# Performance work log

Hardware: AMD Instinct MI355X
Metric: run time of the kernel (lower is better)

The kernel has to match this reference:

```python
import jax, jax.numpy as jnp
import numpy as np

B, C, T = 4, 768, 512
H, KS, NL, W = 12, 3, 6, 4
D = C // H  # 64


def setup_inputs() -> dict:
    key = jax.random.key(0)
    ks = jax.random.split(key, 24)
    def n(k, shape, scale):
        return jax.random.normal(k, shape, dtype=jnp.float32) * scale
    cscale = C ** -0.5
    return {
        "x": jax.random.normal(ks[0], (B, C, T), dtype=jnp.float32),
        "x_mask": jnp.ones((B, 1, T), dtype=jnp.float32),
        "Wq": n(ks[1], (NL, C, C), cscale), "bq": jnp.zeros((NL, C), jnp.float32),
        "Wk": n(ks[2], (NL, C, C), cscale), "bk": jnp.zeros((NL, C), jnp.float32),
        "Wv": n(ks[3], (NL, C, C), cscale), "bv": jnp.zeros((NL, C), jnp.float32),
        "Wo": n(ks[4], (NL, C, C), cscale), "bo": jnp.zeros((NL, C), jnp.float32),
        "emb_rel_k": n(ks[5], (NL, D, 2 * W + 1), D ** -0.5),
        "emb_rel_v": n(ks[6], (NL, D, 2 * W + 1), D ** -0.5),
        "ffn_w1": n(ks[7], (NL, 4 * C, C, KS), (C * KS) ** -0.5),
        "ffn_b1": jnp.zeros((NL, 4 * C), jnp.float32),
        "ffn_w2": n(ks[8], (NL, C, 4 * C, KS), (4 * C * KS) ** -0.5),
        "ffn_b2": jnp.zeros((NL, C), jnp.float32),
        "norm1_g": jnp.ones((NL, C), jnp.float32), "norm1_b": jnp.zeros((NL, C), jnp.float32),
        "norm2_g": jnp.ones((NL, C), jnp.float32), "norm2_b": jnp.zeros((NL, C), jnp.float32),
    }


def _conv1x1(x, w, b):  # x:[B,C,T] w:[O,C] -> [B,O,T]
    return jnp.einsum('oc,bct->bot', w, x) + b[None, :, None]


def _conv1d(x, w, b, pad):  # x:[B,Ci,T] w:[O,Ci,K]
    y = jax.lax.conv_general_dilated(x, w, (1,), [(pad, pad)],
                                     dimension_numbers=('NCH', 'OIH', 'NCH'))
    return y + b[None, :, None]


def _layer_norm_c(x, g, b):  # normalize over channel dim of [B,C,T]
    m = jnp.mean(x, axis=1, keepdims=True)
    v = jnp.var(x, axis=1, keepdims=True)
    return (x - m) * jax.lax.rsqrt(v + 1e-5) * g[None, :, None] + b[None, :, None]


def _rel_to_abs(x):  # [b,h,l,2l-1] -> [b,h,l,l]
    b, h, l, _ = x.shape
    x = jnp.pad(x, ((0, 0), (0, 0), (0, 0), (0, 1)))
    x = x.reshape(b, h, l * 2 * l)
    x = jnp.pad(x, ((0, 0), (0, 0), (0, l - 1)))
    return x.reshape(b, h, l + 1, 2 * l - 1)[:, :, :l, l - 1:]


def _abs_to_rel(x):  # [b,h,l,l] -> [b,h,l,2l-1]
    b, h, l, _ = x.shape
    x = jnp.pad(x, ((0, 0), (0, 0), (0, 0), (0, l - 1)))
    x = x.reshape(b, h, l * l + l * (l - 1))
    x = jnp.pad(x, ((0, 0), (0, 0), (l, 0)))
    return x.reshape(b, h, l, 2 * l)[:, :, :, 1:]


def _get_rel_emb(emb, t, w):  # emb:[D,2w+1] -> [D,2t-1]
    pad = max(t - (w + 1), 0)
    start = max(w + 1 - t, 0)
    e = jnp.pad(emb, ((0, 0), (pad, pad)))
    return e[:, start:start + 2 * t - 1]


def _attention(x, attn_mask, wq, bq, wk, bk, wv, bv, wo, bo, ek, ev):
    b, c, t = x.shape
    scale = D ** 0.5
    q = _conv1x1(x, wq, bq).reshape(b, H, D, t)
    k = _conv1x1(x, wk, bk).reshape(b, H, D, t)
    v = _conv1x1(x, wv, bv).reshape(b, H, D, t)
    scores = jnp.einsum('bhdt,bhds->bhts', q, k) / scale  # [b,H,t,t]
    k_emb = _get_rel_emb(ek, t, W)  # [D,2t-1]
    rel_logits = jnp.einsum('bhdt,dr->bhtr', q / scale, k_emb)
    scores = scores + _rel_to_abs(rel_logits)
    scores = jnp.where(attn_mask == 0, -10000.0, scores)
    p = jax.nn.softmax(scores, axis=-1)
    out = jnp.einsum('bhts,bhds->bhdt', p, v)
    v_emb = _get_rel_emb(ev, t, W)  # [D,2t-1]
    out = out + jnp.einsum('bhtr,dr->bhdt', _abs_to_rel(p), v_emb)
    return _conv1x1(out.reshape(b, c, t), wo, bo)


def _ffn(x, x_mask, w1, b1, w2, b2):
    y = _conv1d(x * x_mask, w1, b1, KS // 2)
    y = jax.nn.gelu(y, approximate=False)
    y = _conv1d(y * x_mask, w2, b2, KS // 2)
    return y * x_mask


def reference(x, x_mask, Wq, bq, Wk, bk, Wv, bv, Wo, bo, emb_rel_k, emb_rel_v,
              ffn_w1, ffn_b1, ffn_w2, ffn_b2, norm1_g, norm1_b, norm2_g, norm2_b):
    attn_mask = x_mask[:, :, None, :] * x_mask[:, :, :, None]  # [B,1,T,T]
    for i in range(NL):
        y = _attention(x, attn_mask, Wq[i], bq[i], Wk[i], bk[i], Wv[i], bv[i],
                       Wo[i], bo[i], emb_rel_k[i], emb_rel_v[i])
        x = _layer_norm_c(x + y, norm1_g[i], norm1_b[i])
        y = _ffn(x, x_mask, ffn_w1[i], ffn_b1[i], ffn_w2[i], ffn_b2[i])
        x = _layer_norm_c(x + y, norm2_g[i], norm2_b[i])
        x = x * x_mask
    return x
```

## Files before the change

kernel.cpp:

```cpp
#include <hip/hip_runtime.h>
#include <cstddef>

namespace {

constexpr int B  = 4;
constexpr int C  = 768;
constexpr int T  = 512;
constexpr int H  = 12;
constexpr int D  = 64;
constexpr int NL = 6;
constexpr int W  = 4;
constexpr int FF = 3072;

typedef __attribute__((ext_vector_type(8))) short sh8;
typedef __attribute__((ext_vector_type(4))) float f32x4;

__device__ inline float gelu_exact(float x) {
  return 0.5f * x * (1.0f + erff(x * 0.70710678118654752440f));
}
__device__ inline unsigned short f2b(float f) {
  unsigned u = __float_as_uint(f);
  unsigned r = (u + 0x7fffu + ((u >> 16) & 1u)) >> 16;
  return (unsigned short)r;
}
__device__ inline float b2f(unsigned short u) {
  return __uint_as_float((unsigned)u << 16);
}
__device__ inline void gload_lds16(const void* g, void* l) {
  __builtin_amdgcn_global_load_lds(
      (const __attribute__((address_space(1))) unsigned int*)g,
      (__attribute__((address_space(3))) unsigned int*)l, 16, 0, 0);
}

__global__ __launch_bounds__(256) void transpose_cvt_in(
    const float* __restrict__ s, unsigned short* __restrict__ dh,
    float* __restrict__ df)
{
  __shared__ float tile[32][33];
  const int b = blockIdx.z;
  const int c0 = blockIdx.y * 32, t0 = blockIdx.x * 32;
  const int tx = threadIdx.x & 31, ty = threadIdx.x >> 5;
  const float* sp = s + ((size_t)b * C + c0) * T + t0;
#pragma unroll
  for (int i = 0; i < 4; ++i)
    tile[ty + i * 8][tx] = sp[(size_t)(ty + i * 8) * T + tx];
  __syncthreads();
  unsigned short* dph = dh + ((size_t)b * T + t0) * C + c0;
  float* dpf = df + ((size_t)b * T + t0) * C + c0;
#pragma unroll
  for (int i = 0; i < 4; ++i) {
    const float v = tile[tx][ty + i * 8];
    dph[(size_t)(ty + i * 8) * C + tx] = f2b(v);
    dpf[(size_t)(ty + i * 8) * C + tx] = v;
  }
}

__global__ __launch_bounds__(256) void transpose_out(
    const float* __restrict__ s, float* __restrict__ d)
{
  __shared__ float tile[32][33];
  const int b = blockIdx.z;
  const int c0 = blockIdx.y * 32, t0 = blockIdx.x * 32;
  const int tx = threadIdx.x & 31, ty = threadIdx.x >> 5;
  const float* sp = s + ((size_t)b * T + t0) * C + c0;
#pragma unroll
  for (int i = 0; i < 4; ++i)
    tile[ty + i * 8][tx] = sp[(size_t)(ty + i * 8) * C + tx];
  __syncthreads();
  float* dp = d + ((size_t)b * C + c0) * T + t0;
#pragma unroll
  for (int i = 0; i < 4; ++i)
    dp[(size_t)(ty + i * 8) * T + tx] = tile[tx][ty + i * 8];
}

__global__ __launch_bounds__(256) void cvt_qkvo_tiled(
    const float* __restrict__ q, const float* __restrict__ k,
    const float* __restrict__ v, const float* __restrict__ o,
    unsigned short* __restrict__ dq, unsigned short* __restrict__ dk,
    unsigned short* __restrict__ dv, unsigned short* __restrict__ dov)
{
  __shared__ float lds[16][132];
  const int z = blockIdx.y;
  const size_t loff = (size_t)blockIdx.z * C * C;
  const float* s = (z == 0 ? q : z == 1 ? k : z == 2 ? v : o) + loff;
  unsigned short* d = (z == 0 ? dq : z == 1 ? dk : z == 2 ? dv : dov) + loff;
  constexpr int KST = C / 32;
  constexpr int KSG = KST / 4;
  const int mt = blockIdx.x / KSG;
  const int ksg = blockIdx.x % KSG;
  const int tid = threadIdx.x;
#pragma unroll
  for (int p = 0; p < 2; ++p) {
    const int f = tid + p * 256;
    const int row = f >> 5, c4 = f & 31;
    f32x4 vv = __builtin_nontemporal_load(
        (const f32x4*)(s + (size_t)(mt * 16 + row) * C + ksg * 128 + c4 * 4));
    *(f32x4*)&lds[row][c4 * 4] = vv;
  }
  __syncthreads();
  const int ksl = tid >> 6, lane = tid & 63;
  const int l15 = lane & 15, lhi = lane >> 4;
  float4 a = *(const float4*)&lds[l15][ksl * 32 + lhi * 8];
  float4 b = *(const float4*)&lds[l15][ksl * 32 + lhi * 8 + 4];
  sh8 u;
  u[0] = (short)f2b(a.x); u[1] = (short)f2b(a.y);
  u[2] = (short)f2b(a.z); u[3] = (short)f2b(a.w);
  u[4] = (short)f2b(b.x); u[5] = (short)f2b(b.y);
  u[6] = (short)f2b(b.z); u[7] = (short)f2b(b.w);
  *(sh8*)(d + ((size_t)(mt * KST + ksg * 4 + ksl) * 64 + lane) * 8) = u;
}

__global__ __launch_bounds__(256) void cvt_ffn_tiled(
    const float* __restrict__ s1, const float* __restrict__ s2,
    unsigned short* __restrict__ d1, unsigned short* __restrict__ d2)
{
  __shared__ float lds[16][388];
  const int z = blockIdx.y;
  const int layer = blockIdx.z;
  const float* src = (z ? s2 : s1) + (size_t)layer * FF * C * 3;
  unsigned short* dst = (z ? d2 : d1) + (size_t)layer * 3 * FF * C;
  const int O  = z ? C : FF;
  const int Ci = z ? FF : C;
  const int KST = Ci >> 5;
  const int KSG = KST >> 2;
  const int mt = blockIdx.x / KSG;
  const int ksg = blockIdx.x % KSG;
  const int tid = threadIdx.x;
  const size_t rowlen = (size_t)Ci * 3;
#pragma unroll
  for (int p = 0; p < 6; ++p) {
    const int f = tid + p * 256;
    const int row = f / 96, c4 = f % 96;
    f32x4 vv = __builtin_nontemporal_load(
        (const f32x4*)(src + (size_t)(mt * 16 + row) * rowlen + ksg * 384 + c4 * 4));
    *(f32x4*)&lds[row][c4 * 4] = vv;
  }
  __syncthreads();
  const int ksl = tid >> 6, lane = tid & 63;
  const int l15 = lane & 15, lhi = lane >> 4;
  const int q0 = ksl * 96 + lhi * 24;
  float f[24];
#pragma unroll
  for (int kq = 0; kq < 6; ++kq) {
    float4 t4 = *(const float4*)&lds[l15][q0 + kq * 4];
    f[kq * 4 + 0] = t4.x; f[kq * 4 + 1] = t4.y;
    f[kq * 4 + 2] = t4.z; f[kq * 4 + 3] = t4.w;
  }
  const size_t fragoff = ((size_t)(mt * KST + ksg * 4 + ksl) * 64 + lane) * 8;
#pragma unroll
  for (int tap = 0; tap < 3; ++tap) {
    sh8 u;
#pragma unroll
    for (int j = 0; j < 8; ++j) u[j] = (short)f2b(f[j * 3 + tap]);
    *(sh8*)(dst + (size_t)tap * O * Ci + fragoff) = u;
  }
}

template <int TAPS, int BN, int KSPLIT, bool GELU, bool MASK_OUT, bool OBF16,
          bool KBIN, bool KBOUT>
__global__ __launch_bounds__(256) void mfma_conv(
    const unsigned short* __restrict__ xin,
    const unsigned short* __restrict__ w0p, const unsigned short* __restrict__ w1p,
    const unsigned short* __restrict__ w2p,
    const float* __restrict__ b0, const float* __restrict__ b1,
    const float* __restrict__ b2,
    const float* __restrict__ mask,
    void* __restrict__ o0p, void* __restrict__ o1p, void* __restrict__ o2p,
    int Cin, int O, int tilesPerPlane, int nz)
{
  constexpr int ROWS_B = BN + TAPS - 1;
  constexpr int PB = 40;
  constexpr int NPASS = BN / 64;
  constexpr int NF = BN / 32;
  constexpr int NT = T / BN;
  __shared__ unsigned short Aw[2][TAPS * 8 * 512];
  __shared__ unsigned short Bx[2][ROWS_B * PB];

  const int nwg = gridDim.x;
  const int orig = blockIdx.x;
  const int wg = (orig & 7) * (nwg >> 3) + (orig >> 3);
  const int txt = wg % NT;
  const int rest = wg / NT;
  const int zz = rest % nz;
  const int ty = rest / nz;

  const int b  = zz / KSPLIT;
  const int kk = zz % KSPLIT;
  const int TOFF = (TAPS == 3) ? -1 : 0;
  const int t0 = txt * BN;
  const int plane = ty / tilesPerPlane;
  const int mt0 = (ty % tilesPerPlane) * 8;
  const int o0 = mt0 * 16;

  const int tid = threadIdx.x;
  const int lane = tid & 63, wid = tid >> 6;
  const int wm = wid >> 1, wn = wid & 1;
  const int l15 = lane & 15, lhi = lane >> 4;
  const int bmask = b * T;

  const unsigned short* wsel = plane == 0 ? w0p : (plane == 1 ? w1p : w2p);
  const float* bp = plane == 0 ? b0 : (plane == 1 ? b1 : b2);

  const int KST = Cin >> 5;
  const int kchunk = KST / KSPLIT;
  const int ks0 = kk * kchunk, ks1 = ks0 + kchunk;
  const int OT = O >> 4;

  const unsigned short* xb_ = xin + (size_t)b * T * Cin;
  const unsigned short* xkb = xin + (size_t)b * KST * T * 32;

  sh8 breg[NPASS], breg2;
  auto stageA = [&](int ks, int buf) {
#pragma unroll
    for (int tap = 0; tap < TAPS; ++tap) {
#pragma unroll
      for (int j = 0; j < 2; ++j) {
        const int rt = wid * 2 + j;
        const unsigned short* src =
            wsel + (((size_t)tap * OT + mt0 + rt) * KST + ks) * 512 + lane * 8;
        gload_lds16(src, &Aw[buf][(tap * 8 + rt) * 512]);
      }
    }
  };
  auto loadB = [&](int ks) {
    const int c0 = ks << 5;
    const unsigned short* kbase = xkb + (size_t)ks * T * 32;
#pragma unroll
    for (int p = 0; p < NPASS; ++p) {
      const int idx = tid + p * 256;
      const int row = idx >> 2, c8 = (idx & 3) << 3;
      const int tsrc = t0 + row + TOFF;
      breg[p] = (sh8)0;
      if ((unsigned)tsrc < (unsigned)T) {
        if constexpr (KBIN)
          breg[p] = *(const sh8*)(kbase + (size_t)tsrc * 32 + c8);
        else
          breg[p] = *(const sh8*)(xb_ + (size_t)tsrc * Cin + c0 + c8);
      }
    }
    if constexpr (TAPS == 3) {
      breg2 = (sh8)0;
      if (tid < 8) {
        const int row = BN + (tid >> 2), c8 = (tid & 3) << 3;
        const int ts2 = t0 + row + TOFF;
        if ((unsigned)ts2 < (unsigned)T) {
          if constexpr (KBIN)
            breg2 = *(const sh8*)(kbase + (size_t)ts2 * 32 + c8);
          else
            breg2 = *(const sh8*)(xb_ + (size_t)ts2 * Cin + c0 + c8);
        }
      }
    }
  };
  auto writeB = [&](int buf) {
#pragma unroll
    for (int p = 0; p < NPASS; ++p) {
      const int idx = tid + p * 256;
      *(sh8*)&Bx[buf][(idx >> 2) * PB + ((idx & 3) << 3)] = breg[p];
    }
    if constexpr (TAPS == 3) {
      if (tid < 8)
        *(sh8*)&Bx[buf][(BN + (tid >> 2)) * PB + ((tid & 3) << 3)] = breg2;
    }
  };

  f32x4 acc[4][NF] = {};

  int cur = 0;
  stageA(ks0, 0);
  loadB(ks0);
  writeB(0);
  __syncthreads();

  for (int ks = ks0; ks < ks1; ++ks) {
    const int nxt = cur ^ 1;
    const bool more = (ks + 1 < ks1);
    if (more) { stageA(ks + 1, nxt); loadB(ks + 1); }
    __builtin_amdgcn_s_setprio(1);
#pragma unroll
    for (int tap = 0; tap < TAPS; ++tap) {
      sh8 af[4], bfr[NF];
#pragma unroll
      for (int m = 0; m < 4; ++m)
        af[m] = *(const sh8*)&Aw[cur][(tap * 8 + wm * 4 + m) * 512 + lane * 8];
#pragma unroll
      for (int n = 0; n < NF; ++n)
        bfr[n] = *(const sh8*)&Bx[cur][(wn * (NF * 16) + n * 16 + l15 + tap) * PB + lhi * 8];
#pragma unroll
      for (int m = 0; m < 4; ++m)
#pragma unroll
        for (int n = 0; n < NF; ++n)
          acc[m][n] = __builtin_amdgcn_mfma_f32_16x16x32_bf16(
              af[m], bfr[n], acc[m][n], 0, 0, 0);
    }
    __builtin_amdgcn_s_setprio(0);
    if (more) writeB(nxt);
    __syncthreads();
    cur = nxt;
  }

  void* obase = plane == 0 ? o0p : (plane == 1 ? o1p : o2p);
  unsigned short* oph = (unsigned short*)obase + (size_t)b * T * O;
  unsigned short* opk = (unsigned short*)obase + (size_t)b * (O >> 5) * T * 32;
  float* opf = (float*)obase + ((size_t)kk * B + b) * (size_t)T * O;
#pragma unroll
  for (int m = 0; m < 4; ++m) {
    const int o = o0 + (wm * 4 + m) * 16 + (lhi << 2);
#pragma unroll
    for (int n = 0; n < NF; ++n) {
      const int t = t0 + wn * (NF * 16) + n * 16 + l15;
      const float mk = MASK_OUT ? mask[bmask + t] : 1.f;
      float v[4];
#pragma unroll
      for (int r4 = 0; r4 < 4; ++r4) {
        float x = acc[m][n][r4];
        if (KSPLIT > 1) {
          if (kk == 0) x += bp[o + r4];
        } else {
          x += bp[o + r4];
        }
        if (GELU) x = gelu_exact(x);
        if (MASK_OUT) x *= mk;
        v[r4] = x;
      }
      if constexpr (OBF16) {
        ushort4 hz;
        hz.x = f2b(v[0]); hz.y = f2b(v[1]); hz.z = f2b(v[2]); hz.w = f2b(v[3]);
        if constexpr (KBOUT)
          *(ushort4*)(opk + ((size_t)(o >> 5) * T + t) * 32 + (o & 31)) = hz;
        else
          *(ushort4*)(oph + (size_t)t * O + o) = hz;
      } else {
        *(float4*)(opf + (size_t)t * O + o) = make_float4(v[0], v[1], v[2], v[3]);
      }
    }
  }
}

__global__ __launch_bounds__(256) void fused_attn(
    const unsigned short* __restrict__ qg,
    const unsigned short* __restrict__ kg,
    const unsigned short* __restrict__ vg,
    const float* __restrict__ mask,
    const float* __restrict__ ek,
    const float* __restrict__ ev,
    unsigned short* __restrict__ outp)
{
  constexpr int PITCH = 72;
  __shared__ unsigned short Qs[64 * PITCH];
  __shared__ unsigned short Ks[2][64 * PITCH];
  __shared__ unsigned short Vs[2][64 * PITCH];
  __shared__ float eks[D * 9], evs[D * 9];
  __shared__ float qekl[64 * 12];
  __shared__ float mks[2][64];
  unsigned short* Ps = Qs;

  const int t0 = blockIdx.x * 64;
  const int bh = blockIdx.y;
  const int b = bh / H, h = bh % H;
  const int tid = threadIdx.x;
  const int lane = tid & 63, w = tid >> 6;
  const int l15 = lane & 15, lhi = lane >> 4;

  const size_t base = (size_t)b * T * C + h * D;
  const unsigned short* qh = qg + base;
  const unsigned short* kh = kg + base;
  const unsigned short* vh = vg + base;

  for (int e = tid; e < D * 9; e += 256) { eks[e] = ek[e]; evs[e] = ev[e]; }
  {
    const int tl = tid & 63, d0 = (tid >> 6) << 4;
    const unsigned short* src = qh + (size_t)(t0 + tl) * C + d0;
    *(sh8*)&Qs[tl * PITCH + d0]     = *(const sh8*)(src);
    *(sh8*)&Qs[tl * PITCH + d0 + 8] = *(const sh8*)(src + 8);
  }
  __syncthreads();
  {
    const int tl = tid & 63, g = tid >> 6;
    for (int j = g; j < 9; j += 4) {
      float a = 0.f;
      for (int d = 0; d < D; ++d)
        a = fmaf(b2f(Qs[tl * PITCH + d]), eks[d * 9 + j], a);
      qekl[tl * 12 + j] = a * 0.125f;
    }
  }
  const int t_loc = w * 16 + l15;
  const int t = t0 + t_loc;
  const float mask_t = mask[b * T + t];
  const sh8 bq0 = *(const sh8*)&Qs[t_loc * PITCH + lhi * 8];
  const sh8 bq1 = *(const sh8*)&Qs[t_loc * PITCH + 32 + lhi * 8];

  const int sl = tid & 63, d0s = (tid >> 6) << 4;
  {
    const unsigned short* srck = kh + (size_t)sl * C + d0s;
    *(sh8*)&Ks[0][sl * PITCH + d0s]     = *(const sh8*)(srck);
    *(sh8*)&Ks[0][sl * PITCH + d0s + 8] = *(const sh8*)(srck + 8);
    const unsigned short* srcv = vh + (size_t)sl * C + d0s;
    sh8 u0 = *(const sh8*)(srcv);
    sh8 u1 = *(const sh8*)(srcv + 8);
#pragma unroll
    for (int j = 0; j < 8; ++j) Vs[0][(d0s + j) * PITCH + sl] = (unsigned short)u0[j];
#pragma unroll
    for (int j = 0; j < 8; ++j) Vs[0][(d0s + 8 + j) * PITCH + sl] = (unsigned short)u1[j];
    if (tid < 64) mks[0][tid] = mask[b * T + tid];
  }
  __syncthreads();

  float m_run = -1e30f, l_run = 0.f;
  f32x4 oacc[4] = {};
  int cur = 0;
  sh8 kr0, kr1, vr0, vr1;
  float mkr = 0.f;

  for (int s0 = 0; s0 < T; s0 += 64) {
    const int nxt = cur ^ 1;
    const bool more = (s0 + 64 < T);
    if (more) {
      const unsigned short* srck = kh + (size_t)(s0 + 64 + sl) * C + d0s;
      kr0 = *(const sh8*)(srck);
      kr1 = *(const sh8*)(srck + 8);
      const unsigned short* srcv = vh + (size_t)(s0 + 64 + sl) * C + d0s;
      vr0 = *(const sh8*)(srcv);
      vr1 = *(const sh8*)(srcv + 8);
      if (tid < 64) mkr = mask[b * T + s0 + 64 + tid];
    }

    float p[16];
#pragma unroll
    for (int n = 0; n < 4; ++n) {
      const sh8 a0 = *(const sh8*)&Ks[cur][(n * 16 + l15) * PITCH + lhi * 8];
      const sh8 a1 = *(const sh8*)&Ks[cur][(n * 16 + l15) * PITCH + 32 + lhi * 8];
      f32x4 acc = {};
      __builtin_amdgcn_s_setprio(1);
      acc = __builtin_amdgcn_mfma_f32_16x16x32_bf16(a0, bq0, acc, 0, 0, 0);
      acc = __builtin_amdgcn_mfma_f32_16x16x32_bf16(a1, bq1, acc, 0, 0, 0);
      __builtin_amdgcn_s_setprio(0);
#pragma unroll
      for (int r = 0; r < 4; ++r) {
        const int s = s0 + n * 16 + lhi * 4 + r;
        float v = acc[r] * 0.125f;
        const int j = s - t + 4;
        if ((unsigned)j < 9u) v += qekl[t_loc * 12 + j];
        if (mask_t * mks[cur][s - s0] == 0.f) v = -10000.0f;
        p[n * 4 + r] = v;
      }
    }
    float mloc = p[0];
#pragma unroll
    for (int i = 1; i < 16; ++i) mloc = fmaxf(mloc, p[i]);
    mloc = fmaxf(mloc, __shfl_xor(mloc, 16));
    mloc = fmaxf(mloc, __shfl_xor(mloc, 32));
    const float m_new = fmaxf(m_run, mloc);
    const float f = __expf(m_run - m_new);
    float sloc = 0.f;
#pragma unroll
    for (int i = 0; i < 16; ++i) { p[i] = __expf(p[i] - m_new); sloc += p[i]; }
    sloc += __shfl_xor(sloc, 16);
    sloc += __shfl_xor(sloc, 32);
    l_run = l_run * f + sloc;
    m_run = m_new;
#pragma unroll
    for (int m = 0; m < 4; ++m)
#pragma unroll
      for (int r = 0; r < 4; ++r) oacc[m][r] *= f;
#pragma unroll
    for (int n = 0; n < 4; ++n) {
      uint2 pk;
      pk.x = (unsigned)f2b(p[n * 4 + 0]) | ((unsigned)f2b(p[n * 4 + 1]) << 16);
      pk.y = (unsigned)f2b(p[n * 4 + 2]) | ((unsigned)f2b(p[n * 4 + 3]) << 16);
      *(uint2*)&Ps[t_loc * PITCH + n * 16 + lhi * 4] = pk;
    }
    asm volatile("s_waitcnt lgkmcnt(0)" ::: "memory");
    const sh8 bp0 = *(const sh8*)&Ps[t_loc * PITCH + lhi * 8];
    const sh8 bp1 = *(const sh8*)&Ps[t_loc * PITCH + 32 + lhi * 8];
    __builtin_amdgcn_s_setprio(1);
#pragma unroll
    for (int m = 0; m < 4; ++m) {
      const sh8 a0 = *(const sh8*)&Vs[cur][(m * 16 + l15) * PITCH + lhi * 8];
      const sh8 a1 = *(const sh8*)&Vs[cur][(m * 16 + l15) * PITCH + 32 + lhi * 8];
      oacc[m] = __builtin_amdgcn_mfma_f32_16x16x32_bf16(a0, bp0, oacc[m], 0, 0, 0);
      oacc[m] = __builtin_amdgcn_mfma_f32_16x16x32_bf16(a1, bp1, oacc[m], 0, 0, 0);
    }
    __builtin_amdgcn_s_setprio(0);
    if (t + 4 >= s0 && t < s0 + 68) {
#pragma unroll
      for (int j = 0; j < 9; ++j) {
        const int s = t + j - 4;
        if (s >= s0 && s < s0 + 64) {
          const float pv = b2f(Ps[t_loc * PITCH + (s - s0)]);
#pragma unroll
          for (int m = 0; m < 4; ++m)
#pragma unroll
            for (int r = 0; r < 4; ++r)
              oacc[m][r] = fmaf(pv, evs[(m * 16 + lhi * 4 + r) * 9 + j], oacc[m][r]);
        }
      }
    }
    if (more) {
      *(sh8*)&Ks[nxt][sl * PITCH + d0s]     = kr0;
      *(sh8*)&Ks[nxt][sl * PITCH + d0s + 8] = kr1;
#pragma unroll
      for (int j = 0; j < 8; ++j) Vs[nxt][(d0s + j) * PITCH + sl] = (unsigned short)vr0[j];
#pragma unroll
      for (int j = 0; j < 8; ++j) Vs[nxt][(d0s + 8 + j) * PITCH + sl] = (unsigned short)vr1[j];
      if (tid < 64) mks[nxt][tid] = mkr;
    }
    __syncthreads();
    cur = nxt;
  }
  const float invl = 1.f / l_run;
  unsigned short* okb = outp + (size_t)b * (C >> 5) * T * 32;
#pragma unroll
  for (int m = 0; m < 4; ++m) {
    ushort4 hz;
    hz.x = f2b(oacc[m][0] * invl);
    hz.y = f2b(oacc[m][1] * invl);
    hz.z = f2b(oacc[m][2] * invl);
    hz.w = f2b(oacc[m][3] * invl);
    const int c = h * D + m * 16 + lhi * 4;
    *(ushort4*)(okb + ((size_t)(c >> 5) * T + t) * 32 + (c & 31)) = hz;
  }
}

template <int NP, bool MASKY, bool MASKF>
__global__ __launch_bounds__(256) void add_norm_wave(
    const float* __restrict__ xr, const float* __restrict__ ypart,
    const float* __restrict__ g, const float* __restrict__ bta,
    const float* __restrict__ mask, float* __restrict__ dst,
    unsigned short* __restrict__ dsth)
{
  const int b = blockIdx.y;
  const int t = blockIdx.x * 4 + (threadIdx.x >> 6);
  const int lane = threadIdx.x & 63;
  const float mkt = mask[b * T + t];
  const size_t rowoff = ((size_t)b * T + t) * C;
  const int ci0 = lane * 12;

  float vv[12];
  float sum = 0.f, sq = 0.f;
#pragma unroll
  for (int q = 0; q < 3; ++q) {
    const int ci = ci0 + q * 4;
    float4 xv = *(const float4*)(xr + rowoff + ci);
    float4 yv = make_float4(0.f, 0.f, 0.f, 0.f);
#pragma unroll
    for (int p = 0; p < NP; ++p) {
      float4 t4 = *(const float4*)(ypart + (size_t)p * B * T * C + rowoff + ci);
      yv.x += t4.x; yv.y += t4.y; yv.z += t4.z; yv.w += t4.w;
    }
    if (MASKY) { yv.x *= mkt; yv.y *= mkt; yv.z *= mkt; yv.w *= mkt; }
    const float v0 = xv.x + yv.x, v1 = xv.y + yv.y;
    const float v2 = xv.z + yv.z, v3 = xv.w + yv.w;
    vv[q * 4 + 0] = v0; vv[q * 4 + 1] = v1; vv[q * 4 + 2] = v2; vv[q * 4 + 3] = v3;
    sum += v0 + v1 + v2 + v3;
    sq = fmaf(v0, v0, fmaf(v1, v1, fmaf(v2, v2, fmaf(v3, v3, sq))));
  }
#pragma unroll
  for (int o = 32; o > 0; o >>= 1) {
    sum += __shfl_xor(sum, o);
    sq += __shfl_xor(sq, o);
  }
  const float m = sum * (1.f / C);
  const float rs = rsqrtf(sq * (1.f / C) - m * m + 1e-5f);
#pragma unroll
  for (int q = 0; q < 3; ++q) {
    const int ci = ci0 + q * 4;
    float4 gv = *(const float4*)(g + ci);
    float4 bv = *(const float4*)(bta + ci);
    float o0 = (vv[q * 4 + 0] - m) * rs * gv.x + bv.x;
    float o1 = (vv[q * 4 + 1] - m) * rs * gv.y + bv.y;
    float o2 = (vv[q * 4 + 2] - m) * rs * gv.z + bv.z;
    float o3 = (vv[q * 4 + 3] - m) * rs * gv.w + bv.w;
    if (MASKF) { o0 *= mkt; o1 *= mkt; o2 *= mkt; o3 *= mkt; }
    *(float4*)(dst + rowoff + ci) = make_float4(o0, o1, o2, o3);
    const float hm = MASKF ? 1.f : mkt;
    ushort4 hz;
    hz.x = f2b(o0 * hm); hz.y = f2b(o1 * hm); hz.z = f2b(o2 * hm); hz.w = f2b(o3 * hm);
    *(ushort4*)(dsth + rowoff + ci) = hz;
  }
}

}

extern "C" void kernel_launch(void* const* d_in, const int* in_sizes, int n_in,
                              void* d_out, int out_size, void* d_ws, size_t ws_size,
                              hipStream_t stream) {
  const float* x_in = (const float*)d_in[0];
  const float* mask = (const float*)d_in[1];
  const float* Wq = (const float*)d_in[2];
  const float* bq = (const float*)d_in[3];
  const float* Wk = (const float*)d_in[4];
  const float* bk = (const float*)d_in[5];
  const float* Wv = (const float*)d_in[6];
  const float* bv = (const float*)d_in[7];
  const float* Wo = (const float*)d_in[8];
  const float* bo = (const float*)d_in[9];
  const float* ek = (const float*)d_in[10];
  const float* ev = (const float*)d_in[11];
  const float* w1 = (const float*)d_in[12];
  const float* b1 = (const float*)d_in[13];
  const float* w2 = (const float*)d_in[14];
  const float* b2 = (const float*)d_in[15];
  const float* n1g = (const float*)d_in[16];
  const float* n1b = (const float*)d_in[17];
  const float* n2g = (const float*)d_in[18];
  const float* n2b = (const float*)d_in[19];

  float* ws = (float*)d_ws;
  const size_t SZ_X = (size_t)B * C * T;
  const size_t SZ_W1 = (size_t)3 * FF * C;
  float* xr    = ws;
  float* xr1   = xr + SZ_X;
  float* ypart = xr1 + SZ_X;
  unsigned short* xbh = (unsigned short*)(ypart + 4 * SZ_X);
  unsigned short* xfh = xbh + SZ_X;
  unsigned short* qbh = xfh + SZ_X;
  unsigned short* kbh = qbh + SZ_X;
  unsigned short* vbh = kbh + SZ_X;
  unsigned short* hidh = vbh + SZ_X;
  unsigned short* w1t = hidh + (size_t)B * FF * T;
  unsigned short* w2t = w1t + (size_t)NL * SZ_W1;
  unsigned short* wqt = w2t + (size_t)NL * SZ_W1;
  unsigned short* wkt = wqt + (size_t)NL * C * C;
  unsigned short* wvt = wkt + (size_t)NL * C * C;
  unsigned short* wot = wvt + (size_t)NL * C * C;
  float* outp = (float*)d_out;

  const dim3 blk(256);
  transpose_cvt_in<<<dim3(T / 32, C / 32, B), blk, 0, stream>>>(x_in, xbh, xr);
  cvt_qkvo_tiled<<<dim3((C / 16) * (C / 128), 4, NL), blk, 0, stream>>>(
      Wq, Wk, Wv, Wo, wqt, wkt, wvt, wot);
  cvt_ffn_tiled<<<dim3((FF / 16) * (C / 128), 2, NL), blk, 0, stream>>>(
      w1, w2, w1t, w2t);

  for (int i = 0; i < NL; ++i) {
    const size_t wOff = (size_t)i * C * C;
    const unsigned short* w1l = w1t + (size_t)i * SZ_W1;
    const unsigned short* w2l = w2t + (size_t)i * SZ_W1;
    mfma_conv<1, 64, 1, false, false, true, false, false>
        <<<dim3(8 * 18 * 4), blk, 0, stream>>>(
        xbh, wqt + wOff, wkt + wOff, wvt + wOff,
        bq + i * C, bk + i * C, bv + i * C, mask,
        qbh, kbh, vbh, C, C, 6, 4);
    fused_attn<<<dim3(T / 64, B * H), blk, 0, stream>>>(
        qbh, kbh, vbh, mask, ek + (size_t)i * D * 9, ev + (size_t)i * D * 9, hidh);
    mfma_conv<1, 64, 3, false, false, false, true, false>
        <<<dim3(8 * 6 * 12), blk, 0, stream>>>(
        hidh, wot + wOff, wot + wOff, wot + wOff,
        bo + i * C, bo + i * C, bo + i * C, mask,
        ypart, ypart, ypart, C, C, 6, 12);
    add_norm_wave<3, false, false><<<dim3(T / 4, B), blk, 0, stream>>>(
        xr, ypart, n1g + i * C, n1b + i * C, mask, xr1, xfh);
    mfma_conv<3, 128, 1, true, true, true, false, true>
        <<<dim3(4 * 24 * 4), blk, 0, stream>>>(
        xfh, w1l, w1l, w1l, b1 + i * FF, b1 + i * FF, b1 + i * FF, mask,
        hidh, hidh, hidh, C, FF, 24, 4);
    mfma_conv<3, 128, 4, false, false, false, true, false>
        <<<dim3(4 * 6 * 16), blk, 0, stream>>>(
        hidh, w2l, w2l, w2l, b2 + i * C, b2 + i * C, b2 + i * C, mask,
        ypart, ypart, ypart, FF, C, 6, 16);
    add_norm_wave<4, true, true><<<dim3(T / 4, B), blk, 0, stream>>>(
        xr1, ypart, n2g + i * C, n2b + i * C, mask, xr, xbh);
  }
  transpose_out<<<dim3(T / 32, C / 32, B), blk, 0, stream>>>(xr, outp);
}
```

Before: 1.105 ms.

## Load conv B fragments directly from global into registers, drop LDS staging

Result: slower. 1.743 ms (+57.8%).

```diff
diff --git a/kernel.cpp b/kernel.cpp
--- a/kernel.cpp
+++ b/kernel.cpp
@@ -168,13 +168,9 @@
     void* __restrict__ o0p, void* __restrict__ o1p, void* __restrict__ o2p,
     int Cin, int O, int tilesPerPlane, int nz)
 {
-  constexpr int ROWS_B = BN + TAPS - 1;
-  constexpr int PB = 40;
-  constexpr int NPASS = BN / 64;
   constexpr int NF = BN / 32;
   constexpr int NT = T / BN;
   __shared__ unsigned short Aw[2][TAPS * 8 * 512];
-  __shared__ unsigned short Bx[2][ROWS_B * PB];
 
   const int nwg = gridDim.x;
   const int orig = blockIdx.x;
@@ -186,7 +182,6 @@
 
   const int b  = zz / KSPLIT;
   const int kk = zz % KSPLIT;
-  const int TOFF = (TAPS == 3) ? -1 : 0;
   const int t0 = txt * BN;
   const int plane = ty / tilesPerPlane;
   const int mt0 = (ty % tilesPerPlane) * 8;
@@ -209,7 +204,8 @@
   const unsigned short* xb_ = xin + (size_t)b * T * Cin;
   const unsigned short* xkb = xin + (size_t)b * KST * T * 32;
 
-  sh8 breg[NPASS], breg2;
+  const int trow0 = t0 + wn * (NF * 16) + l15 + ((TAPS == 3) ? -1 : 0);
+
   auto stageA = [&](int ks, int buf) {
 #pragma unroll
     for (int tap = 0; tap < TAPS; ++tap) {
@@ -222,81 +218,55 @@
       }
     }
   };
-  auto loadB = [&](int ks) {
-    const int c0 = ks << 5;
-    const unsigned short* kbase = xkb + (size_t)ks * T * 32;
-#pragma unroll
-    for (int p = 0; p < NPASS; ++p) {
-      const int idx = tid + p * 256;
-      const int row = idx >> 2, c8 = (idx & 3) << 3;
-      const int tsrc = t0 + row + TOFF;
-      breg[p] = (sh8)0;
-      if ((unsigned)tsrc < (unsigned)T) {
-        if constexpr (KBIN)
-          breg[p] = *(const sh8*)(kbase + (size_t)tsrc * 32 + c8);
-        else
-          breg[p] = *(const sh8*)(xb_ + (size_t)tsrc * Cin + c0 + c8);
+  auto loadBall = [&](int ks, sh8* dst) {
+#pragma unroll
+    for (int tap = 0; tap < TAPS; ++tap)
+#pragma unroll
+      for (int n = 0; n < NF; ++n) {
+        const int tl = trow0 + tap + n * 16;
+        sh8 v = (sh8)0;
+        if (TAPS == 1 || (unsigned)tl < (unsigned)T) {
+          const unsigned short* p = KBIN
+              ? xkb + ((size_t)ks * T + tl) * 32 + lhi * 8
+              : xb_ + (size_t)tl * Cin + (ks << 5) + lhi * 8;
+          v = *(const sh8*)p;
+        }
+        dst[tap * NF + n] = v;
       }
-    }
-    if constexpr (TAPS == 3) {
-      breg2 = (sh8)0;
-      if (tid < 8) {
-        const int row = BN + (tid >> 2), c8 = (tid & 3) << 3;
-        const int ts2 = t0 + row + TOFF;
-        if ((unsigned)ts2 < (unsigned)T) {
-          if constexpr (KBIN)
-            breg2 = *(const sh8*)(kbase + (size_t)ts2 * 32 + c8);
-          else
-            breg2 = *(const sh8*)(xb_ + (size_t)ts2 * Cin + c0 + c8);
-        }
-      }
-    }
   };
-  auto writeB = [&](int buf) {
-#pragma unroll
-    for (int p = 0; p < NPASS; ++p) {
-      const int idx = tid + p * 256;
-      *(sh8*)&Bx[buf][(idx >> 2) * PB + ((idx & 3) << 3)] = breg[p];
-    }
-    if constexpr (TAPS == 3) {
-      if (tid < 8)
-        *(sh8*)&Bx[buf][(BN + (tid >> 2)) * PB + ((tid & 3) << 3)] = breg2;
-    }
-  };
 
   f32x4 acc[4][NF] = {};
-
-  int cur = 0;
-  stageA(ks0, 0);
-  loadB(ks0);
-  writeB(0);
-  __syncthreads();
-
-  for (int ks = ks0; ks < ks1; ++ks) {
-    const int nxt = cur ^ 1;
-    const bool more = (ks + 1 < ks1);
-    if (more) { stageA(ks + 1, nxt); loadB(ks + 1); }
-    __builtin_amdgcn_s_setprio(1);
+  sh8 B0[TAPS * NF], B1[TAPS * NF];
+
+  auto compute = [&](int abuf, const sh8* bset) {
 #pragma unroll
     for (int tap = 0; tap < TAPS; ++tap) {
-      sh8 af[4], bfr[NF];
+      sh8 af[4];
 #pragma unroll
       for (int m = 0; m < 4; ++m)
-        af[m] = *(const sh8*)&Aw[cur][(tap * 8 + wm * 4 + m) * 512 + lane * 8];
-#pragma unroll
-      for (int n = 0; n < NF; ++n)
-        bfr[n] = *(const sh8*)&Bx[cur][(wn * (NF * 16) + n * 16 + l15 + tap) * PB + lhi * 8];
+        af[m] = *(const sh8*)&Aw[abuf][(tap * 8 + wm * 4 + m) * 512 + lane * 8];
 #pragma unroll
       for (int m = 0; m < 4; ++m)
 #pragma unroll
         for (int n = 0; n < NF; ++n)
           acc[m][n] = __builtin_amdgcn_mfma_f32_16x16x32_bf16(
-              af[m], bfr[n], acc[m][n], 0, 0, 0);
-    }
-    __builtin_amdgcn_s_setprio(0);
-    if (more) writeB(nxt);
+              af[m], bset[tap * NF + n], acc[m][n], 0, 0, 0);
+    }
+  };
+
+  stageA(ks0, 0);
+  loadBall(ks0, B0);
+  __syncthreads();
+
+  for (int ks = ks0; ks < ks1; ks += 2) {
+    stageA(ks + 1, 1);
+    loadBall(ks + 1, B1);
+    compute(0, B0);
     __syncthreads();
-    cur = nxt;
+    const bool more2 = (ks + 2 < ks1);
+    if (more2) { stageA(ks + 2, 0); loadBall(ks + 2, B0); }
+    compute(1, B1);
+    __syncthreads();
   }
 
   void* obase = plane == 0 ? o0p : (plane == 1 ? o1p : o2p);
```
